# Optimization experiments

Measured on AMD Instinct MI355X. Metric: run time of the kernel, lower is better.

Reference implementation:

```python
import jax, jax.numpy as jnp
import numpy as np

B, D, N, R = 2048, 6, 256, 16


def setup_inputs() -> dict:
    key = jax.random.key(0)
    k_x, k_L, k_q, k_k, k_v, k_o = jax.random.split(key, 6)
    return {
        "x": jax.random.normal(k_x, (B, D, N), dtype=jnp.float32),
        "L": jax.random.normal(k_L, (B, N, N), dtype=jnp.float32),
        "Aq": jax.random.normal(k_q, (R, D), dtype=jnp.float32),
        "Ak": jax.random.normal(k_k, (R, D), dtype=jnp.float32),
        "Av": jax.random.normal(k_v, (R, D), dtype=jnp.float32),
        "Ao": jax.random.normal(k_o, (1, R), dtype=jnp.float32),
    }


def reference(x, L, Aq, Ak, Av, Ao):
    # numNeighbors: count of entries >= 1 in row 0 of each sample's L, plus 1
    numN = jnp.sum((L[:, 0, :] >= 1).astype(jnp.float32), axis=1).reshape(-1, 1, 1) + 1.0  # [B,1,1]
    # Q/K/V projections with tanh: [r,d] x [B,d,N] -> [B,r,N]
    Q = jnp.tanh(jnp.einsum("rd,bdn->brn", Aq, x))
    K = jnp.tanh(jnp.einsum("rd,bdn->brn", Ak, x))
    V = jnp.tanh(jnp.einsum("rd,bdn->brn", Av, x))
    # attention over the small r x r score matrix, scaled by sqrt(neighbor count)
    scores = jnp.einsum("brn,bsn->brs", Q, K) / jnp.sqrt(numN)  # [B,r,r]
    attn = jax.nn.softmax(scores, axis=2)
    o = jnp.einsum("brs,bsn->brn", attn, V)  # [B,r,N]
    H = jax.nn.silu(jnp.einsum("or,brn->bon", Ao, o))[:, 0, :]  # [B,N]
    return (jnp.sum(H, axis=1) ** 2)[:, None]  # [B,1]
```

## Files before the change

### kernel.cpp

```cpp
#include <hip/hip_runtime.h>

namespace {

constexpr int Dd = 6;
constexpr int Nn = 256;
constexpr int Rr = 16;

typedef __attribute__((ext_vector_type(8))) short bf16x8;
typedef __attribute__((ext_vector_type(4))) float f32x4;
typedef __attribute__((ext_vector_type(4))) int i32x4;

__device__ __forceinline__ float fast_tanh(float xv) {
  float e = __builtin_amdgcn_exp2f(xv * 2.8853900817779268f);
  return fmaf(-2.0f, __builtin_amdgcn_rcpf(e + 1.0f), 1.0f);
}

__device__ __forceinline__ unsigned pack_bf16(float a, float b) {
  unsigned r;
  asm("v_cvt_pk_bf16_f32 %0, %1, %2" : "=v"(r) : "v"(a), "v"(b));
  return r;
}

__global__ __launch_bounds__(128, 4) void att_h_fused(
    const float* __restrict__ x,
    const float* __restrict__ L,
    const float* __restrict__ Aq,
    const float* __restrict__ Ak,
    const float* __restrict__ Av,
    const float* __restrict__ Ao,
    float* __restrict__ out)
{
  __shared__ __align__(16) float xs[2][Dd][128];
  __shared__ __align__(16) f32x4 accbuf[2][64];
  __shared__ float hs[2];

  const int b    = blockIdx.x;
  const int tid  = threadIdx.x;
  const int h    = tid >> 6;
  const int lane = tid & 63;

  const float* xb = x + (size_t)b * (Dd * Nn);

#pragma unroll
  for (int i = 0; i < 3; ++i) {
    const int d = 2 * i + (lane >> 5);
    const int c = (lane & 31) * 4;
    *(float4*)&xs[h][d][c] = *(const float4*)(xb + d * Nn + h * 128 + c);
  }

  const float4 lr = *(const float4*)(L + (size_t)b * Nn * Nn + lane * 4);
  float cnt = (float)(lr.x >= 1.0f) + (float)(lr.y >= 1.0f) +
              (float)(lr.z >= 1.0f) + (float)(lr.w >= 1.0f);
#pragma unroll
  for (int o = 1; o < 64; o <<= 1) cnt += __shfl_xor(cnt, o);
  const float scale = rsqrtf(cnt + 1.0f);

  const int r     = lane & 15;
  const int quart = lane >> 4;
  float aqr[Dd], akr[Dd];
#pragma unroll
  for (int p = 0; p < 3; ++p) {
    const float2 a = *(const float2*)(Aq + r * Dd + 2 * p);
    const float2 c = *(const float2*)(Ak + r * Dd + 2 * p);
    aqr[2 * p] = a.x; aqr[2 * p + 1] = a.y;
    akr[2 * p] = c.x; akr[2 * p + 1] = c.y;
  }

  f32x4 acc0 = {0.f, 0.f, 0.f, 0.f}, acc1 = {0.f, 0.f, 0.f, 0.f};
#pragma unroll 2
  for (int kb = 0; kb < 4; ++kb) {
    const int nw = kb * 32 + quart * 8;
    float xa[Dd][8];
#pragma unroll
    for (int d = 0; d < Dd; ++d) {
      const float4 t0 = *(const float4*)&xs[h][d][nw];
      const float4 t1 = *(const float4*)&xs[h][d][nw + 4];
      xa[d][0] = t0.x; xa[d][1] = t0.y; xa[d][2] = t0.z; xa[d][3] = t0.w;
      xa[d][4] = t1.x; xa[d][5] = t1.y; xa[d][6] = t1.z; xa[d][7] = t1.w;
    }
    float qv[8], kv[8];
#pragma unroll
    for (int j = 0; j < 8; ++j) {
      float aq = 0.0f, ak = 0.0f;
#pragma unroll
      for (int d = 0; d < Dd; ++d) {
        aq = fmaf(aqr[d], xa[d][j], aq);
        ak = fmaf(akr[d], xa[d][j], ak);
      }
      qv[j] = fast_tanh(aq);
      kv[j] = fast_tanh(ak);
    }
    i32x4 qp, kp;
#pragma unroll
    for (int p = 0; p < 4; ++p) {
      qp[p] = (int)pack_bf16(qv[2 * p], qv[2 * p + 1]);
      kp[p] = (int)pack_bf16(kv[2 * p], kv[2 * p + 1]);
    }
    const bf16x8 qa = __builtin_bit_cast(bf16x8, qp);
    const bf16x8 ka = __builtin_bit_cast(bf16x8, kp);
    if (kb & 1)
      acc1 = __builtin_amdgcn_mfma_f32_16x16x32_bf16(qa, ka, acc1, 0, 0, 0);
    else
      acc0 = __builtin_amdgcn_mfma_f32_16x16x32_bf16(qa, ka, acc0, 0, 0, 0);
  }

  accbuf[h][lane] = acc0 + acc1;
  __syncthreads();
  const f32x4 other = accbuf[1 - h][lane];
  const f32x4 acc   = acc0 + acc1 + other;

  const float4 ao4 = *(const float4*)(Ao + quart * 4);
  const float aoarr[4] = {ao4.x, ao4.y, ao4.z, ao4.w};
  float wp = 0.0f;
#pragma unroll
  for (int j = 0; j < 4; ++j) {
    const float sc = acc[j] * scale;
    float mj = sc;
#pragma unroll
    for (int o = 1; o < 16; o <<= 1) mj = fmaxf(mj, __shfl_xor(mj, o));
    const float ej = __builtin_amdgcn_exp2f((sc - mj) * 1.4426950408889634f);
    float sj = ej;
#pragma unroll
    for (int o = 1; o < 16; o <<= 1) sj += __shfl_xor(sj, o);
    wp = fmaf(aoarr[j], ej * __builtin_amdgcn_rcpf(sj), wp);
  }
  wp += __shfl_xor(wp, 16);
  wp += __shfl_xor(wp, 32);
  float wb[Rr];
#pragma unroll
  for (int s = 0; s < Rr; ++s) wb[s] = __shfl(wp, s);

  float hsum = 0.0f;
#pragma unroll
  for (int c = 0; c < 2; ++c) {
    float xcv[Dd];
#pragma unroll
    for (int d = 0; d < Dd; ++d) xcv[d] = xs[h][d][lane * 2 + c];
    float hv = 0.0f;
#pragma unroll
    for (int s = 0; s < Rr; ++s) {
      float av = 0.0f;
#pragma unroll
      for (int d = 0; d < Dd; ++d) av = fmaf(Av[s * Dd + d], xcv[d], av);
      hv = fmaf(wb[s], fast_tanh(av), hv);
    }
    hsum += hv * __builtin_amdgcn_rcpf(
                     1.0f + __builtin_amdgcn_exp2f(-1.4426950408889634f * hv));
  }
#pragma unroll
  for (int o = 1; o < 64; o <<= 1) hsum += __shfl_xor(hsum, o);
  if (lane == 0) hs[h] = hsum;
  __syncthreads();
  if (tid == 0) {
    const float tot = hs[0] + hs[1];
    out[b] = tot * tot;
  }
}

}

extern "C" void kernel_launch(void* const* d_in, const int* in_sizes, int n_in,
                              void* d_out, int out_size, void* d_ws, size_t ws_size,
                              hipStream_t stream) {
  const float* x  = (const float*)d_in[0];
  const float* L  = (const float*)d_in[1];
  const float* Aq = (const float*)d_in[2];
  const float* Ak = (const float*)d_in[3];
  const float* Av = (const float*)d_in[4];
  const float* Ao = (const float*)d_in[5];
  float* out = (float*)d_out;

  const int B = in_sizes[0] / (Dd * Nn);
  att_h_fused<<<dim3(B), dim3(128), 0, stream>>>(x, L, Aq, Ak, Av, Ao, out);
}
```

Before: 17.17 us.

## Split each sample across four waves instead of two

Each block now runs 256 threads, so every wave covers 64 of the 256 columns instead of 128. The x tile becomes one shared [D][N] array loaded with float2, and the four partial score accumulators are summed through shared memory. The projection loop is also reordered so it accumulates over d for eight columns at once. The aim is more parallelism per sample and less serial work per wave, at the cost of more threads per block and larger cross-wave reductions.

```diff
diff --git a/kernel.cpp b/kernel.cpp
--- a/kernel.cpp
+++ b/kernel.cpp
@@ -21,7 +21,7 @@
   return r;
 }
 
-__global__ __launch_bounds__(128, 4) void att_h_fused(
+__global__ __launch_bounds__(256, 6) void att_h_fused(
     const float* __restrict__ x,
     const float* __restrict__ L,
     const float* __restrict__ Aq,
@@ -30,22 +30,24 @@
     const float* __restrict__ Ao,
     float* __restrict__ out)
 {
-  __shared__ __align__(16) float xs[2][Dd][128];
-  __shared__ __align__(16) f32x4 accbuf[2][64];
-  __shared__ float hs[2];
+  __shared__ __align__(16) float xs[Dd][Nn];
+  __shared__ __align__(16) f32x4 accbuf[4][64];
+  __shared__ float hs[4];
 
   const int b    = blockIdx.x;
   const int tid  = threadIdx.x;
-  const int h    = tid >> 6;
+  const int w    = tid >> 6;
   const int lane = tid & 63;
 
   const float* xb = x + (size_t)b * (Dd * Nn);
 
+  {
+    const int c = (lane & 31) * 2 + w * 64;
 #pragma unroll
-  for (int i = 0; i < 3; ++i) {
-    const int d = 2 * i + (lane >> 5);
-    const int c = (lane & 31) * 4;
-    *(float4*)&xs[h][d][c] = *(const float4*)(xb + d * Nn + h * 128 + c);
+    for (int i = 0; i < 3; ++i) {
+      const int d = 2 * i + (lane >> 5);
+      *(float2*)&xs[d][c] = *(const float2*)(xb + d * Nn + c);
+    }
   }
 
   const float4 lr = *(const float4*)(L + (size_t)b * Nn * Nn + lane * 4);
@@ -67,34 +69,27 @@
   }
 
   f32x4 acc0 = {0.f, 0.f, 0.f, 0.f}, acc1 = {0.f, 0.f, 0.f, 0.f};
-#pragma unroll 2
-  for (int kb = 0; kb < 4; ++kb) {
-    const int nw = kb * 32 + quart * 8;
-    float xa[Dd][8];
+#pragma unroll
+  for (int kb = 0; kb < 2; ++kb) {
+    const int nw = w * 64 + kb * 32 + quart * 8;
+    float aq[8] = {0.f, 0.f, 0.f, 0.f, 0.f, 0.f, 0.f, 0.f};
+    float ak[8] = {0.f, 0.f, 0.f, 0.f, 0.f, 0.f, 0.f, 0.f};
 #pragma unroll
     for (int d = 0; d < Dd; ++d) {
-      const float4 t0 = *(const float4*)&xs[h][d][nw];
-      const float4 t1 = *(const float4*)&xs[h][d][nw + 4];
-      xa[d][0] = t0.x; xa[d][1] = t0.y; xa[d][2] = t0.z; xa[d][3] = t0.w;
-      xa[d][4] = t1.x; xa[d][5] = t1.y; xa[d][6] = t1.z; xa[d][7] = t1.w;
-    }
-    float qv[8], kv[8];
+      const float4 t0 = *(const float4*)&xs[d][nw];
+      const float4 t1 = *(const float4*)&xs[d][nw + 4];
+      const float xv[8] = {t0.x, t0.y, t0.z, t0.w, t1.x, t1.y, t1.z, t1.w};
 #pragma unroll
-    for (int j = 0; j < 8; ++j) {
-      float aq = 0.0f, ak = 0.0f;
-#pragma unroll
-      for (int d = 0; d < Dd; ++d) {
-        aq = fmaf(aqr[d], xa[d][j], aq);
-        ak = fmaf(akr[d], xa[d][j], ak);
+      for (int j = 0; j < 8; ++j) {
+        aq[j] = fmaf(aqr[d], xv[j], aq[j]);
+        ak[j] = fmaf(akr[d], xv[j], ak[j]);
       }
-      qv[j] = fast_tanh(aq);
-      kv[j] = fast_tanh(ak);
     }
     i32x4 qp, kp;
 #pragma unroll
     for (int p = 0; p < 4; ++p) {
-      qp[p] = (int)pack_bf16(qv[2 * p], qv[2 * p + 1]);
-      kp[p] = (int)pack_bf16(kv[2 * p], kv[2 * p + 1]);
+      qp[p] = (int)pack_bf16(fast_tanh(aq[2 * p]), fast_tanh(aq[2 * p + 1]));
+      kp[p] = (int)pack_bf16(fast_tanh(ak[2 * p]), fast_tanh(ak[2 * p + 1]));
     }
     const bf16x8 qa = __builtin_bit_cast(bf16x8, qp);
     const bf16x8 ka = __builtin_bit_cast(bf16x8, kp);
@@ -104,10 +99,10 @@
       acc0 = __builtin_amdgcn_mfma_f32_16x16x32_bf16(qa, ka, acc0, 0, 0, 0);
   }
 
-  accbuf[h][lane] = acc0 + acc1;
+  accbuf[w][lane] = acc0 + acc1;
   __syncthreads();
-  const f32x4 other = accbuf[1 - h][lane];
-  const f32x4 acc   = acc0 + acc1 + other;
+  f32x4 acc = accbuf[0][lane] + accbuf[1][lane];
+  acc += accbuf[2][lane] + accbuf[3][lane];
 
   const float4 ao4 = *(const float4*)(Ao + quart * 4);
   const float aoarr[4] = {ao4.x, ao4.y, ao4.z, ao4.w};
@@ -130,29 +125,25 @@
 #pragma unroll
   for (int s = 0; s < Rr; ++s) wb[s] = __shfl(wp, s);
 
-  float hsum = 0.0f;
+  float xcv[Dd];
 #pragma unroll
-  for (int c = 0; c < 2; ++c) {
-    float xcv[Dd];
+  for (int d = 0; d < Dd; ++d) xcv[d] = xs[d][w * 64 + lane];
+  float hv = 0.0f;
 #pragma unroll
-    for (int d = 0; d < Dd; ++d) xcv[d] = xs[h][d][lane * 2 + c];
-    float hv = 0.0f;
+  for (int s = 0; s < Rr; ++s) {
+    float av = 0.0f;
 #pragma unroll
-    for (int s = 0; s < Rr; ++s) {
-      float av = 0.0f;
-#pragma unroll
-      for (int d = 0; d < Dd; ++d) av = fmaf(Av[s * Dd + d], xcv[d], av);
-      hv = fmaf(wb[s], fast_tanh(av), hv);
-    }
-    hsum += hv * __builtin_amdgcn_rcpf(
-                     1.0f + __builtin_amdgcn_exp2f(-1.4426950408889634f * hv));
+    for (int d = 0; d < Dd; ++d) av = fmaf(Av[s * Dd + d], xcv[d], av);
+    hv = fmaf(wb[s], fast_tanh(av), hv);
   }
+  float hsum = hv * __builtin_amdgcn_rcpf(
+                        1.0f + __builtin_amdgcn_exp2f(-1.4426950408889634f * hv));
 #pragma unroll
   for (int o = 1; o < 64; o <<= 1) hsum += __shfl_xor(hsum, o);
-  if (lane == 0) hs[h] = hsum;
+  if (lane == 0) hs[w] = hsum;
   __syncthreads();
   if (tid == 0) {
-    const float tot = hs[0] + hs[1];
+    const float tot = hs[0] + hs[1] + hs[2] + hs[3];
     out[b] = tot * tot;
   }
 }
@@ -171,5 +162,5 @@
   float* out = (float*)d_out;
 
   const int B = in_sizes[0] / (Dd * Nn);
-  att_h_fused<<<dim3(B), dim3(128), 0, stream>>>(x, L, Aq, Ak, Av, Ao, out);
+  att_h_fused<<<dim3(B), dim3(256), 0, stream>>>(x, L, Aq, Ak, Av, Ao, out);
 }
```

Measured after the change: 16.90 us. About the same (-1.6%).
